# Kernel tuning notes

Hardware: AMD Instinct MI355X
Metric: run time of the kernel (lower is better)

Reference implementation:

```python
import jax, jax.numpy as jnp
import numpy as np


def setup_inputs() -> dict:
    key = jax.random.key(0)
    k1, k2 = jax.random.split(key)
    decoder_state = jax.random.normal(k1, (64, 1024), dtype=jnp.float32)
    encoder_outputs = jax.random.normal(k2, (64, 2048, 1024), dtype=jnp.float32)
    return {"decoder_state": decoder_state, "encoder_outputs": encoder_outputs}


def reference(decoder_state, encoder_outputs):
    # scores[b, i] = s_t . h_i  -> [B, S]
    scores = jnp.einsum('bh,bsh->bs', decoder_state, encoder_outputs)
    attn_weights = jax.nn.softmax(scores, axis=1)            # [B, S]
    # context[b] = sum_i a[b,i] * h_i -> [B, H]
    context = jnp.einsum('bs,bsh->bh', attn_weights, encoder_outputs)
    return context, attn_weights
```

## Files before the change

### kernel.cpp

```cpp
#include <hip/hip_runtime.h>
#include <math.h>

#define BATCH 64
#define SEQ   2048
#define HID   1024
#define CHUNKS 16
#define ROWS_PER_BLOCK (SEQ / CHUNKS)
#define NWAVES 4
#define ROWS_PER_WAVE (ROWS_PER_BLOCK / NWAVES)
#define PART_STRIDE 1028

__global__ __launch_bounds__(256) void attn_pass1(
    const float* __restrict__ dec, const float* __restrict__ enc,
    float* __restrict__ scores, float* __restrict__ partials)
{
    const int b     = blockIdx.x / CHUNKS;
    const int chunk = blockIdx.x % CHUNKS;
    const int tid   = threadIdx.x;
    const int wave  = tid >> 6;
    const int lane  = tid & 63;

    const float4* decv = reinterpret_cast<const float4*>(dec + b * HID);
    float4 sv[4];
#pragma unroll
    for (int p = 0; p < 4; ++p) sv[p] = decv[p * 64 + lane];

    float m = -1e30f, l = 0.0f;
    float4 c[4];
#pragma unroll
    for (int p = 0; p < 4; ++p) c[p] = make_float4(0.f, 0.f, 0.f, 0.f);

    const int row0 = chunk * ROWS_PER_BLOCK + wave * ROWS_PER_WAVE;
    const float4* encv = reinterpret_cast<const float4*>(enc + (size_t)b * SEQ * HID);

    for (int r = 0; r < ROWS_PER_WAVE; ++r) {
        const int i = row0 + r;
        const float4* rowp = encv + (size_t)i * (HID / 4);
        float4 e[4];
#pragma unroll
        for (int p = 0; p < 4; ++p) e[p] = rowp[p * 64 + lane];

        float dot = 0.f;
#pragma unroll
        for (int p = 0; p < 4; ++p)
            dot += e[p].x * sv[p].x + e[p].y * sv[p].y + e[p].z * sv[p].z + e[p].w * sv[p].w;
#pragma unroll
        for (int off = 32; off > 0; off >>= 1) dot += __shfl_xor(dot, off, 64);

        if (lane == 0) scores[b * SEQ + i] = dot;

        const float mn    = fmaxf(m, dot);
        const float scale = __expf(m - mn);
        const float pw    = __expf(dot - mn);
        l = l * scale + pw;
        m = mn;
#pragma unroll
        for (int p = 0; p < 4; ++p) {
            c[p].x = c[p].x * scale + pw * e[p].x;
            c[p].y = c[p].y * scale + pw * e[p].y;
            c[p].z = c[p].z * scale + pw * e[p].z;
            c[p].w = c[p].w * scale + pw * e[p].w;
        }
    }

    __shared__ float lm[NWAVES], ll[NWAVES];
    __shared__ float lc[NWAVES][HID];
    float4* lcw = reinterpret_cast<float4*>(lc[wave]);
#pragma unroll
    for (int p = 0; p < 4; ++p) lcw[p * 64 + lane] = c[p];
    if (lane == 0) { lm[wave] = m; ll[wave] = l; }
    __syncthreads();

    const float M = fmaxf(fmaxf(lm[0], lm[1]), fmaxf(lm[2], lm[3]));
    float w[NWAVES];
    float L = 0.f;
#pragma unroll
    for (int k = 0; k < NWAVES; ++k) { w[k] = __expf(lm[k] - M); L += ll[k] * w[k]; }

    float4 acc = make_float4(0.f, 0.f, 0.f, 0.f);
#pragma unroll
    for (int k = 0; k < NWAVES; ++k) {
        float4 v = reinterpret_cast<const float4*>(lc[k])[tid];
        acc.x += v.x * w[k]; acc.y += v.y * w[k];
        acc.z += v.z * w[k]; acc.w += v.w * w[k];
    }
    float* rec = partials + (size_t)blockIdx.x * PART_STRIDE;
    reinterpret_cast<float4*>(rec)[tid] = acc;
    if (tid == 0) { rec[HID] = M; rec[HID + 1] = L; }
}

__global__ __launch_bounds__(256) void attn_pass2(
    const float* __restrict__ scores, const float* __restrict__ partials,
    float* __restrict__ out_ctx, float* __restrict__ out_attn)
{
    const int b = blockIdx.x;
    const int t = threadIdx.x;

    float mk[CHUNKS], lk[CHUNKS];
    float M = -1e30f;
#pragma unroll
    for (int k = 0; k < CHUNKS; ++k) {
        const float* rec = partials + (size_t)(b * CHUNKS + k) * PART_STRIDE;
        mk[k] = rec[HID];
        lk[k] = rec[HID + 1];
        M = fmaxf(M, mk[k]);
    }
    float L = 0.f;
    float wk[CHUNKS];
#pragma unroll
    for (int k = 0; k < CHUNKS; ++k) { wk[k] = __expf(mk[k] - M); L += lk[k] * wk[k]; }
    const float invL = 1.0f / L;

    float4 acc = make_float4(0.f, 0.f, 0.f, 0.f);
#pragma unroll
    for (int k = 0; k < CHUNKS; ++k) {
        const float4* rec4 =
            reinterpret_cast<const float4*>(partials + (size_t)(b * CHUNKS + k) * PART_STRIDE);
        float4 v = rec4[t];
        acc.x += v.x * wk[k]; acc.y += v.y * wk[k];
        acc.z += v.z * wk[k]; acc.w += v.w * wk[k];
    }
    float4 o;
    o.x = acc.x * invL; o.y = acc.y * invL; o.z = acc.z * invL; o.w = acc.w * invL;
    reinterpret_cast<float4*>(out_ctx + b * HID)[t] = o;

    for (int i = t; i < SEQ; i += 256) {
        out_attn[b * SEQ + i] = __expf(scores[b * SEQ + i] - M) * invL;
    }
}

extern "C" void kernel_launch(void* const* d_in, const int* in_sizes, int n_in,
                              void* d_out, int out_size, void* d_ws, size_t ws_size,
                              hipStream_t stream) {
    const float* dec = (const float*)d_in[0];
    const float* enc = (const float*)d_in[1];
    float* out = (float*)d_out;

    float* scores   = (float*)d_ws;
    float* partials = scores + BATCH * SEQ;

    attn_pass1<<<BATCH * CHUNKS, 256, 0, stream>>>(dec, enc, scores, partials);
    attn_pass2<<<BATCH, 256, 0, stream>>>(scores, partials, out, out + BATCH * HID);
}
```

Measured before the change: 117.7 us.

## Double-buffer encoder row loads with nontemporal hints and branchy online softmax

The pass-1 loop now prefetches the next encoder row into a second register buffer while the current row is processed, so global load latency overlaps the dot-product reduction. Loads use nontemporal hints because the 512 MB encoder tensor is streamed once. The online-softmax update is split by branch so the common case (no new max) skips one exp and the rescale multiply. Launch bounds add an occupancy hint, at the cost of more registers for the extra row buffer.

Result: faster. 100.4 us (-14.7%).

```diff
diff --git a/kernel.cpp b/kernel.cpp
--- a/kernel.cpp
+++ b/kernel.cpp
@@ -10,7 +10,9 @@
 #define ROWS_PER_WAVE (ROWS_PER_BLOCK / NWAVES)
 #define PART_STRIDE 1028
 
-__global__ __launch_bounds__(256) void attn_pass1(
+typedef float f32x4 __attribute__((ext_vector_type(4)));
+
+__global__ __launch_bounds__(256, 4) void attn_pass1(
     const float* __restrict__ dec, const float* __restrict__ enc,
     float* __restrict__ scores, float* __restrict__ partials)
 {
@@ -20,52 +22,69 @@
     const int wave  = tid >> 6;
     const int lane  = tid & 63;
 
-    const float4* decv = reinterpret_cast<const float4*>(dec + b * HID);
-    float4 sv[4];
+    const f32x4* decv = reinterpret_cast<const f32x4*>(dec + b * HID);
+    f32x4 sv[4];
 #pragma unroll
     for (int p = 0; p < 4; ++p) sv[p] = decv[p * 64 + lane];
 
     float m = -1e30f, l = 0.0f;
-    float4 c[4];
+    f32x4 c[4];
 #pragma unroll
-    for (int p = 0; p < 4; ++p) c[p] = make_float4(0.f, 0.f, 0.f, 0.f);
+    for (int p = 0; p < 4; ++p) c[p] = (f32x4)(0.0f);
 
     const int row0 = chunk * ROWS_PER_BLOCK + wave * ROWS_PER_WAVE;
-    const float4* encv = reinterpret_cast<const float4*>(enc + (size_t)b * SEQ * HID);
+    const f32x4* rowp = reinterpret_cast<const f32x4*>(enc + (size_t)b * SEQ * HID)
+                        + (size_t)row0 * (HID / 4) + lane;
 
-    for (int r = 0; r < ROWS_PER_WAVE; ++r) {
-        const int i = row0 + r;
-        const float4* rowp = encv + (size_t)i * (HID / 4);
-        float4 e[4];
+    f32x4 eA[4], eB[4];
 #pragma unroll
-        for (int p = 0; p < 4; ++p) e[p] = rowp[p * 64 + lane];
+    for (int p = 0; p < 4; ++p) eA[p] = __builtin_nontemporal_load(rowp + p * 64);
 
+    auto process = [&](const f32x4 (&e)[4], int r) {
         float dot = 0.f;
 #pragma unroll
-        for (int p = 0; p < 4; ++p)
-            dot += e[p].x * sv[p].x + e[p].y * sv[p].y + e[p].z * sv[p].z + e[p].w * sv[p].w;
+        for (int p = 0; p < 4; ++p) {
+            dot += e[p].x * sv[p].x; dot += e[p].y * sv[p].y;
+            dot += e[p].z * sv[p].z; dot += e[p].w * sv[p].w;
+        }
 #pragma unroll
         for (int off = 32; off > 0; off >>= 1) dot += __shfl_xor(dot, off, 64);
 
-        if (lane == 0) scores[b * SEQ + i] = dot;
+        if (lane == 0) scores[b * SEQ + row0 + r] = dot;
 
-        const float mn    = fmaxf(m, dot);
-        const float scale = __expf(m - mn);
-        const float pw    = __expf(dot - mn);
-        l = l * scale + pw;
-        m = mn;
+        if (dot <= m) {
+            const float pw = __expf(dot - m);
+            l += pw;
 #pragma unroll
-        for (int p = 0; p < 4; ++p) {
-            c[p].x = c[p].x * scale + pw * e[p].x;
-            c[p].y = c[p].y * scale + pw * e[p].y;
-            c[p].z = c[p].z * scale + pw * e[p].z;
-            c[p].w = c[p].w * scale + pw * e[p].w;
+            for (int p = 0; p < 4; ++p) c[p] += pw * e[p];
+        } else {
+            const float sc = __expf(m - dot);
+            l = l * sc + 1.0f;
+#pragma unroll
+            for (int p = 0; p < 4; ++p) c[p] = c[p] * sc + e[p];
+            m = dot;
         }
+    };
+
+    for (int r = 0; r < ROWS_PER_WAVE; r += 2) {
+        const f32x4* rp1 = rowp + (size_t)(r + 1) * (HID / 4);
+#pragma unroll
+        for (int p = 0; p < 4; ++p) eB[p] = __builtin_nontemporal_load(rp1 + p * 64);
+
+        process(eA, r);
+
+        if (r + 2 < ROWS_PER_WAVE) {
+            const f32x4* rp2 = rowp + (size_t)(r + 2) * (HID / 4);
+#pragma unroll
+            for (int p = 0; p < 4; ++p) eA[p] = __builtin_nontemporal_load(rp2 + p * 64);
+        }
+
+        process(eB, r + 1);
     }
 
     __shared__ float lm[NWAVES], ll[NWAVES];
     __shared__ float lc[NWAVES][HID];
-    float4* lcw = reinterpret_cast<float4*>(lc[wave]);
+    f32x4* lcw = reinterpret_cast<f32x4*>(lc[wave]);
 #pragma unroll
     for (int p = 0; p < 4; ++p) lcw[p * 64 + lane] = c[p];
     if (lane == 0) { lm[wave] = m; ll[wave] = l; }
@@ -77,15 +96,14 @@
 #pragma unroll
     for (int k = 0; k < NWAVES; ++k) { w[k] = __expf(lm[k] - M); L += ll[k] * w[k]; }
 
-    float4 acc = make_float4(0.f, 0.f, 0.f, 0.f);
+    f32x4 acc = (f32x4)(0.0f);
 #pragma unroll
     for (int k = 0; k < NWAVES; ++k) {
-        float4 v = reinterpret_cast<const float4*>(lc[k])[tid];
-        acc.x += v.x * w[k]; acc.y += v.y * w[k];
-        acc.z += v.z * w[k]; acc.w += v.w * w[k];
+        f32x4 v = reinterpret_cast<const f32x4*>(lc[k])[tid];
+        acc += v * w[k];
     }
     float* rec = partials + (size_t)blockIdx.x * PART_STRIDE;
-    reinterpret_cast<float4*>(rec)[tid] = acc;
+    reinterpret_cast<f32x4*>(rec)[tid] = acc;
     if (tid == 0) { rec[HID] = M; rec[HID + 1] = L; }
 }
 
@@ -111,18 +129,15 @@
     for (int k = 0; k < CHUNKS; ++k) { wk[k] = __expf(mk[k] - M); L += lk[k] * wk[k]; }
     const float invL = 1.0f / L;
 
-    float4 acc = make_float4(0.f, 0.f, 0.f, 0.f);
+    f32x4 acc = (f32x4)(0.0f);
 #pragma unroll
     for (int k = 0; k < CHUNKS; ++k) {
-        const float4* rec4 =
-            reinterpret_cast<const float4*>(partials + (size_t)(b * CHUNKS + k) * PART_STRIDE);
-        float4 v = rec4[t];
-        acc.x += v.x * wk[k]; acc.y += v.y * wk[k];
-        acc.z += v.z * wk[k]; acc.w += v.w * wk[k];
+        const f32x4* rec4 =
+            reinterpret_cast<const f32x4*>(partials + (size_t)(b * CHUNKS + k) * PART_STRIDE);
+        acc += rec4[t] * wk[k];
     }
-    float4 o;
-    o.x = acc.x * invL; o.y = acc.y * invL; o.z = acc.z * invL; o.w = acc.w * invL;
-    reinterpret_cast<float4*>(out_ctx + b * HID)[t] = o;
+    acc *= invL;
+    reinterpret_cast<f32x4*>(out_ctx + b * HID)[t] = acc;
 
     for (int i = t; i < SEQ; i += 256) {
         out_attn[b * SEQ + i] = __expf(scores[b * SEQ + i] - M) * invL;
```
